# Kernel optimization log

Hardware: AMD Instinct MI355X
Metric: run time of the kernel (lower is better)

The kernel has to match this reference:

```python
import jax, jax.numpy as jnp
import numpy as np

E = 8          # num_experts
K = 2          # num_experts_per_tok
D = 1024       # d_model
F = 4096       # d_ff


def setup_inputs() -> dict:
    key = jax.random.key(0)
    k1, k2, k3, k4, k5 = jax.random.split(key, 5)
    s = 0.02
    return {
        "x": jax.random.normal(k1, (2, 2048, D), dtype=jnp.float32),
        "gate_w": jax.random.normal(k2, (D, E), dtype=jnp.float32) * s,
        "w1": jax.random.normal(k3, (E, D, F), dtype=jnp.float32) * s,
        "w2": jax.random.normal(k4, (E, F, D), dtype=jnp.float32) * s,
        "w3": jax.random.normal(k5, (E, D, F), dtype=jnp.float32) * s,
    }


def reference(x, gate_w, w1, w2, w3):
    # x: [B, S, D] -> squash to tokens [T, D]
    xs = x.reshape(-1, x.shape[-1])                      # [T, D]
    gate_logits = xs @ gate_w                            # [T, E]
    topw, sel = jax.lax.top_k(gate_logits, K)            # [T, K] each
    # softmax over the K selected logits in float32, cast back (matches torch code)
    topw = jax.nn.softmax(topw.astype(jnp.float32), axis=-1).astype(x.dtype)
    # per-token combine weight for every expert: zero where not selected [T, E]
    comb = (jax.nn.one_hot(sel, E, dtype=x.dtype) * topw[..., None]).sum(axis=1)
    out = jnp.zeros_like(xs)
    # loop over fixed small expert count (structurally distinct weights);
    # masked-dense combine is mathematically identical to the gather/scatter
    # in the original (weight is exactly 0 for unselected tokens)
    for i in range(E):
        h = jax.nn.silu(xs @ w1[i]) * (xs @ w3[i])       # [T, F] SwiGLU
        out = out + comb[:, i:i + 1] * (h @ w2[i])       # [T, D]
    return out.reshape(x.shape)
```

## Files before the change

### kernel.cpp

```cpp
#include <hip/hip_runtime.h>


#define T_TOK 4096
#define DM    1024
#define FF    4096
#define NE    8

#define BM 128
#define BN 128
#define BK 32
#define BS 36

typedef unsigned short u16;
typedef short short8 __attribute__((ext_vector_type(8)));
typedef float floatx4 __attribute__((ext_vector_type(4)));

#define WS_COUNTS  0u
#define WS_CURS    32u
#define WS_OFFS    64u
#define WS_SEL     4096u
#define WS_SELW    (4096u + 32768u)
#define WS_STOK    (4096u + 65536u)
#define WS_SW      (4096u + 98304u)
#define WS_XBF     (1u << 20)
#define WS_HBUF    ((1u << 20) + (8u << 20))

__device__ __forceinline__ u16 f2bf(float f) {
  union { float f; unsigned int u; } v; v.f = f;
  unsigned int r = v.u + 0x7fffu + ((v.u >> 16) & 1u);
  return (u16)(r >> 16);
}

__device__ __forceinline__ short8 ld_b_frag(const u16* p) {
  union { unsigned long long q[2]; short8 v; } r;
  r.q[0] = *(const unsigned long long*)(p);
  r.q[1] = *(const unsigned long long*)(p + 4);
  return r.v;
}

__global__ __launch_bounds__(256) void gate_kernel(
    const float* __restrict__ x, const float* __restrict__ gw,
    u16* __restrict__ xbf, int* __restrict__ sel, float* __restrict__ selw,
    int* __restrict__ counts)
{
  const int t = blockIdx.x * 4 + (threadIdx.x >> 6);
  const int lane = threadIdx.x & 63;
  const float* xr = x + (size_t)t * DM;
  double acc[NE];
#pragma unroll
  for (int e = 0; e < NE; ++e) acc[e] = 0.0;
#pragma unroll 4
  for (int i = 0; i < 16; ++i) {
    const int d = i * 64 + lane;
    const float xv = xr[d];
    xbf[(size_t)t * DM + d] = f2bf(xv);
    const float4* g = (const float4*)(gw + (size_t)d * NE);
    float4 g0 = g[0], g1 = g[1];
    acc[0] += (double)xv * g0.x; acc[1] += (double)xv * g0.y;
    acc[2] += (double)xv * g0.z; acc[3] += (double)xv * g0.w;
    acc[4] += (double)xv * g1.x; acc[5] += (double)xv * g1.y;
    acc[6] += (double)xv * g1.z; acc[7] += (double)xv * g1.w;
  }
#pragma unroll
  for (int off = 32; off >= 1; off >>= 1) {
#pragma unroll
    for (int e = 0; e < NE; ++e) acc[e] += __shfl_xor(acc[e], off, 64);
  }
  if (lane == 0) {
    int i1 = 0; double v1 = acc[0];
#pragma unroll
    for (int e = 1; e < NE; ++e) if (acc[e] > v1) { v1 = acc[e]; i1 = e; }
    int i2 = -1; double v2 = -1e300;
#pragma unroll
    for (int e = 0; e < NE; ++e) if (e != i1 && acc[e] > v2) { v2 = acc[e]; i2 = e; }
    float p1 = 1.0f / (1.0f + expf((float)(v2 - v1)));
    sel[t * 2] = i1; sel[t * 2 + 1] = i2;
    selw[t * 2] = p1; selw[t * 2 + 1] = 1.0f - p1;
    atomicAdd(&counts[i1], 1);
    atomicAdd(&counts[i2], 1);
  }
}

__global__ void offsets_kernel(const int* __restrict__ counts, int* __restrict__ offsets) {
  if (threadIdx.x == 0) {
    int s = 0;
#pragma unroll
    for (int e = 0; e < NE; ++e) { offsets[e] = s; s += counts[e]; }
  }
}

__global__ void fill_kernel(const int* __restrict__ sel, const float* __restrict__ selw,
                            const int* __restrict__ offsets, int* __restrict__ cursors,
                            int* __restrict__ stok, float* __restrict__ sw)
{
  const int t = blockIdx.x * blockDim.x + threadIdx.x;
  if (t >= T_TOK) return;
#pragma unroll
  for (int k = 0; k < 2; ++k) {
    int e = sel[t * 2 + k];
    int pos = atomicAdd(&cursors[e], 1);
    int p = offsets[e] + pos;
    stok[p] = t;
    sw[p] = selw[t * 2 + k];
  }
}

__global__ __launch_bounds__(256, 2) void gemm1_kernel(
    const u16* __restrict__ xbf, const float* __restrict__ w1, const float* __restrict__ w3,
    const int* __restrict__ stok, const int* __restrict__ offsets,
    const int* __restrict__ counts, u16* __restrict__ Hbuf)
{
  const int e  = blockIdx.z;
  const int mt = blockIdx.y;
  const int ne = counts[e];
  if (mt * BM >= ne) return;
  const int nt = blockIdx.x;
  const int base = offsets[e];
  const float* __restrict__ W1 = w1 + (size_t)e * DM * FF;
  const float* __restrict__ W3 = w3 + (size_t)e * DM * FF;

  __shared__ u16 Al[BM][BK];
  __shared__ u16 B1l[BN][BS];
  __shared__ u16 B3l[BN][BS];

  const int tid  = threadIdx.x;
  const int lane = tid & 63;
  const int wv   = tid >> 6;
  const int wm   = (wv & 1) * 64;
  const int wn   = (wv >> 1) * 64;
  const int ln15 = lane & 15;
  const int q    = lane >> 4;

  const int arow = tid >> 1;
  const int aseg = (tid & 1) * 16;
  const int rg_a = mt * BM + arow;
  const u16* asrc = nullptr;
  if (rg_a < ne) {
    int tok = stok[base + rg_a];
    asrc = xbf + (size_t)tok * DM + aseg;
  }

  const int nb = tid & 127;
  const int kh = (tid >> 7) * 16;
  const int n0 = nt * BN;
  const float* b1p = W1 + (size_t)kh * FF + n0 + nb;
  const float* b3p = W3 + (size_t)kh * FF + n0 + nb;

  floatx4 acc1[4][4], acc3[4][4];
#pragma unroll
  for (int mi = 0; mi < 4; ++mi)
#pragma unroll
    for (int ni = 0; ni < 4; ++ni) {
      acc1[mi][ni] = (floatx4){0.f, 0.f, 0.f, 0.f};
      acc3[mi][ni] = (floatx4){0.f, 0.f, 0.f, 0.f};
    }

  for (int kc = 0; kc < DM; kc += BK) {
    if (asrc) {
      const uint4* s = (const uint4*)(asrc + kc);
      *(uint4*)&Al[arow][aseg]     = s[0];
      *(uint4*)&Al[arow][aseg + 8] = s[1];
    } else {
      uint4 z = {0u, 0u, 0u, 0u};
      *(uint4*)&Al[arow][aseg]     = z;
      *(uint4*)&Al[arow][aseg + 8] = z;
    }
    const float* p1 = b1p + (size_t)kc * FF;
    const float* p3 = b3p + (size_t)kc * FF;
#pragma unroll
    for (int kk = 0; kk < 16; kk += 4) {
      union { u16 s[4]; uint2 u; } v1, v3;
#pragma unroll
      for (int j = 0; j < 4; ++j) {
        v1.s[j] = f2bf(p1[(size_t)(kk + j) * FF]);
        v3.s[j] = f2bf(p3[(size_t)(kk + j) * FF]);
      }
      *(uint2*)&B1l[nb][kh + kk] = v1.u;
      *(uint2*)&B3l[nb][kh + kk] = v3.u;
    }
    __syncthreads();

    short8 af[4];
#pragma unroll
    for (int mi = 0; mi < 4; ++mi)
      af[mi] = *(const short8*)&Al[wm + mi * 16 + ln15][q * 8];
#pragma unroll
    for (int ni = 0; ni < 4; ++ni) {
      short8 b1 = ld_b_frag(&B1l[wn + ni * 16 + ln15][q * 8]);
      short8 b3 = ld_b_frag(&B3l[wn + ni * 16 + ln15][q * 8]);
#pragma unroll
      for (int mi = 0; mi < 4; ++mi) {
        acc1[mi][ni] = __builtin_amdgcn_mfma_f32_16x16x32_bf16(af[mi], b1, acc1[mi][ni], 0, 0, 0);
        acc3[mi][ni] = __builtin_amdgcn_mfma_f32_16x16x32_bf16(af[mi], b3, acc3[mi][ni], 0, 0, 0);
      }
    }
    __syncthreads();
  }

#pragma unroll
  for (int mi = 0; mi < 4; ++mi) {
#pragma unroll
    for (int reg = 0; reg < 4; ++reg) {
      int rg = mt * BM + wm + mi * 16 + q * 4 + reg;
      if (rg < ne) {
        u16* dst = Hbuf + (size_t)(base + rg) * FF + n0 + wn + ln15;
#pragma unroll
        for (int ni = 0; ni < 4; ++ni) {
          float a = acc1[mi][ni][reg];
          float b = acc3[mi][ni][reg];
          float h = (a / (1.0f + __expf(-a))) * b;
          dst[ni * 16] = f2bf(h);
        }
      }
    }
  }
}

__global__ __launch_bounds__(256, 2) void gemm2_kernel(
    const u16* __restrict__ Hbuf, const float* __restrict__ w2,
    const int* __restrict__ stok, const float* __restrict__ sw,
    const int* __restrict__ offsets, const int* __restrict__ counts,
    float* __restrict__ out)
{
  const int e  = blockIdx.z;
  const int mt = blockIdx.y;
  const int ne = counts[e];
  if (mt * BM >= ne) return;
  const int nt = blockIdx.x;
  const int base = offsets[e];
  const float* __restrict__ W2 = w2 + (size_t)e * FF * DM;

  __shared__ u16 Al[BM][BK];
  __shared__ u16 Bl[BN][BS];

  const int tid  = threadIdx.x;
  const int lane = tid & 63;
  const int wv   = tid >> 6;
  const int wm   = (wv & 1) * 64;
  const int wn   = (wv >> 1) * 64;
  const int ln15 = lane & 15;
  const int q    = lane >> 4;

  const int arow = tid >> 1;
  const int aseg = (tid & 1) * 16;
  const int rg_a = mt * BM + arow;
  const u16* asrc = nullptr;
  if (rg_a < ne) asrc = Hbuf + (size_t)(base + rg_a) * FF + aseg;

  const int nb = tid & 127;
  const int kh = (tid >> 7) * 16;
  const int n0 = nt * BN;
  const float* bp = W2 + (size_t)kh * DM + n0 + nb;

  floatx4 acc[4][4];
#pragma unroll
  for (int mi = 0; mi < 4; ++mi)
#pragma unroll
    for (int ni = 0; ni < 4; ++ni) acc[mi][ni] = (floatx4){0.f, 0.f, 0.f, 0.f};

  for (int kc = 0; kc < FF; kc += BK) {
    if (asrc) {
      const uint4* s = (const uint4*)(asrc + kc);
      *(uint4*)&Al[arow][aseg]     = s[0];
      *(uint4*)&Al[arow][aseg + 8] = s[1];
    } else {
      uint4 z = {0u, 0u, 0u, 0u};
      *(uint4*)&Al[arow][aseg]     = z;
      *(uint4*)&Al[arow][aseg + 8] = z;
    }
    const float* p2 = bp + (size_t)kc * DM;
#pragma unroll
    for (int kk = 0; kk < 16; kk += 4) {
      union { u16 s[4]; uint2 u; } v2;
#pragma unroll
      for (int j = 0; j < 4; ++j) v2.s[j] = f2bf(p2[(size_t)(kk + j) * DM]);
      *(uint2*)&Bl[nb][kh + kk] = v2.u;
    }
    __syncthreads();

    short8 af[4];
#pragma unroll
    for (int mi = 0; mi < 4; ++mi)
      af[mi] = *(const short8*)&Al[wm + mi * 16 + ln15][q * 8];
#pragma unroll
    for (int ni = 0; ni < 4; ++ni) {
      short8 b = ld_b_frag(&Bl[wn + ni * 16 + ln15][q * 8]);
#pragma unroll
      for (int mi = 0; mi < 4; ++mi)
        acc[mi][ni] = __builtin_amdgcn_mfma_f32_16x16x32_bf16(af[mi], b, acc[mi][ni], 0, 0, 0);
    }
    __syncthreads();
  }

#pragma unroll
  for (int mi = 0; mi < 4; ++mi) {
#pragma unroll
    for (int reg = 0; reg < 4; ++reg) {
      int rg = mt * BM + wm + mi * 16 + q * 4 + reg;
      if (rg < ne) {
        int p = base + rg;
        int tok = stok[p];
        float wgt = sw[p];
        float* dst = out + (size_t)tok * DM + n0 + wn + ln15;
#pragma unroll
        for (int ni = 0; ni < 4; ++ni)
          atomicAdd(&dst[ni * 16], wgt * acc[mi][ni][reg]);
      }
    }
  }
}

extern "C" void kernel_launch(void* const* d_in, const int* in_sizes, int n_in,
                              void* d_out, int out_size, void* d_ws, size_t ws_size,
                              hipStream_t stream) {
  const float* x  = (const float*)d_in[0];
  const float* gw = (const float*)d_in[1];
  const float* w1 = (const float*)d_in[2];
  const float* w2 = (const float*)d_in[3];
  const float* w3 = (const float*)d_in[4];
  float* out = (float*)d_out;
  char* ws = (char*)d_ws;

  int*   counts  = (int*)(ws + WS_COUNTS);
  int*   cursors = (int*)(ws + WS_CURS);
  int*   offsets = (int*)(ws + WS_OFFS);
  int*   sel     = (int*)(ws + WS_SEL);
  float* selw    = (float*)(ws + WS_SELW);
  int*   stok    = (int*)(ws + WS_STOK);
  float* sw      = (float*)(ws + WS_SW);
  u16*   xbf     = (u16*)(ws + WS_XBF);
  u16*   Hbuf    = (u16*)(ws + WS_HBUF);

  size_t need = (size_t)WS_HBUF + (size_t)(T_TOK * 2) * FF * 2;
  if (ws_size < need) return;

  hipMemsetAsync(ws, 0, 96, stream);
  hipMemsetAsync(d_out, 0, (size_t)T_TOK * DM * sizeof(float), stream);

  gate_kernel<<<T_TOK / 4, 256, 0, stream>>>(x, gw, xbf, sel, selw, counts);
  offsets_kernel<<<1, 64, 0, stream>>>(counts, offsets);
  fill_kernel<<<T_TOK / 256, 256, 0, stream>>>(sel, selw, offsets, cursors, stok, sw);
  gemm1_kernel<<<dim3(FF / BN, T_TOK / BM, NE), 256, 0, stream>>>(xbf, w1, w3, stok, offsets, counts, Hbuf);
  gemm2_kernel<<<dim3(DM / BN, T_TOK / BM, NE), 256, 0, stream>>>(Hbuf, w2, stok, sw, offsets, counts, out);
}
```

Measured before the change: 1.050 ms.

## Pre-transpose weights to bf16 and stream tiles via async global-to-LDS loads

Adds a conversion pass that transposes and casts w1, w3 and w2 to bf16 K-major layouts in the workspace each call. New GEMM kernels then copy A and B tiles straight into LDS with global_load_lds, with no per-thread fp32-to-bf16 conversion or transposed staging. The aim is to halve weight bytes read inside the GEMMs and simplify the load path. The cost is an extra read of all fp32 weights plus a bf16 write every call. The new loop also has no double buffering and may have LDS bank conflicts. The old path is kept as a fallback when the workspace is too small.

```diff
diff --git a/kernel.cpp b/kernel.cpp
--- a/kernel.cpp
+++ b/kernel.cpp
@@ -22,13 +22,22 @@
 #define WS_SELW    (4096u + 32768u)
 #define WS_STOK    (4096u + 65536u)
 #define WS_SW      (4096u + 98304u)
-#define WS_XBF     (1u << 20)
-#define WS_HBUF    ((1u << 20) + (8u << 20))
+#define WS_XBF     ((size_t)1 << 20)
+#define WS_HBUF    ((size_t)9 << 20)
+#define WS_WT1     ((size_t)73 << 20)
+#define WS_WT3     ((size_t)137 << 20)
+#define WS_WT2     ((size_t)201 << 20)
 
 __device__ __forceinline__ u16 f2bf(float f) {
   union { float f; unsigned int u; } v; v.f = f;
   unsigned int r = v.u + 0x7fffu + ((v.u >> 16) & 1u);
   return (u16)(r >> 16);
+}
+
+__device__ __forceinline__ void async16(u16* lds, const u16* g) {
+  __builtin_amdgcn_global_load_lds(
+      (const __attribute__((address_space(1))) unsigned int*)g,
+      (__attribute__((address_space(3))) unsigned int*)lds, 16, 0, 0);
 }
 
 __device__ __forceinline__ short8 ld_b_frag(const u16* p) {
@@ -105,6 +114,215 @@
   }
 }
 
+__global__ __launch_bounds__(256) void convt_kernel(const float* __restrict__ src,
+                                                    u16* __restrict__ dst, int K, int N)
+{
+  __shared__ float tile[64][65];
+  const int e = blockIdx.z;
+  src += (size_t)e * K * N;
+  dst += (size_t)e * K * N;
+  const int n0 = blockIdx.x * 64;
+  const int k0 = blockIdx.y * 64;
+  const int tr = threadIdx.x >> 4;
+  const int tc = (threadIdx.x & 15) * 4;
+#pragma unroll
+  for (int i = 0; i < 64; i += 16) {
+    const float4 v = *(const float4*)&src[(size_t)(k0 + tr + i) * N + n0 + tc];
+    tile[tr + i][tc]     = v.x; tile[tr + i][tc + 1] = v.y;
+    tile[tr + i][tc + 2] = v.z; tile[tr + i][tc + 3] = v.w;
+  }
+  __syncthreads();
+#pragma unroll
+  for (int i = 0; i < 64; i += 16) {
+    union { u16 s[4]; uint2 u; } o;
+#pragma unroll
+    for (int j = 0; j < 4; ++j) o.s[j] = f2bf(tile[tc + j][tr + i]);
+    *(uint2*)&dst[(size_t)(n0 + tr + i) * K + k0 + tc] = o.u;
+  }
+}
+
+__global__ __launch_bounds__(256, 2) void gemm1p_kernel(
+    const u16* __restrict__ xbf, const u16* __restrict__ wt1, const u16* __restrict__ wt3,
+    const int* __restrict__ stok, const int* __restrict__ offsets,
+    const int* __restrict__ counts, u16* __restrict__ Hbuf)
+{
+  const int e  = blockIdx.z;
+  const int mt = blockIdx.y;
+  const int ne = counts[e];
+  if (mt * BM >= ne) return;
+  const int nt = blockIdx.x;
+  const int base = offsets[e];
+  const u16* __restrict__ W1 = wt1 + (size_t)e * DM * FF;
+  const u16* __restrict__ W3 = wt3 + (size_t)e * DM * FF;
+
+  __shared__ u16 Al[BM * BK];
+  __shared__ u16 B1l[BN * BK];
+  __shared__ u16 B3l[BN * BK];
+
+  const int tid  = threadIdx.x;
+  const int lane = tid & 63;
+  const int wv   = tid >> 6;
+  const int wm   = (wv & 1) * 64;
+  const int wn   = (wv >> 1) * 64;
+  const int ln15 = lane & 15;
+  const int q    = lane >> 4;
+  const int n0   = nt * BN;
+
+  const int rsub = lane >> 2;
+  const int seg  = (lane & 3) * 8;
+
+  const u16* ag[2]; const u16* b1g[2]; const u16* b3g[2];
+#pragma unroll
+  for (int it = 0; it < 2; ++it) {
+    int r  = wv * 32 + it * 16 + rsub;
+    int rg = mt * BM + r;
+    int p  = base + (rg < ne ? rg : 0);
+    int tok = stok[p];
+    ag[it]  = xbf + (size_t)tok * DM + seg;
+    int n   = n0 + r;
+    b1g[it] = W1 + (size_t)n * DM + seg;
+    b3g[it] = W3 + (size_t)n * DM + seg;
+  }
+  u16* al[2]  = { Al  + (wv * 32) * BK, Al  + (wv * 32 + 16) * BK };
+  u16* b1l[2] = { B1l + (wv * 32) * BK, B1l + (wv * 32 + 16) * BK };
+  u16* b3l[2] = { B3l + (wv * 32) * BK, B3l + (wv * 32 + 16) * BK };
+
+  floatx4 acc1[4][4], acc3[4][4];
+#pragma unroll
+  for (int mi = 0; mi < 4; ++mi)
+#pragma unroll
+    for (int ni = 0; ni < 4; ++ni) {
+      acc1[mi][ni] = (floatx4){0.f, 0.f, 0.f, 0.f};
+      acc3[mi][ni] = (floatx4){0.f, 0.f, 0.f, 0.f};
+    }
+
+  for (int kc = 0; kc < DM; kc += BK) {
+    async16(al[0],  ag[0]  + kc); async16(al[1],  ag[1]  + kc);
+    async16(b1l[0], b1g[0] + kc); async16(b1l[1], b1g[1] + kc);
+    async16(b3l[0], b3g[0] + kc); async16(b3l[1], b3g[1] + kc);
+    __syncthreads();
+
+    short8 af[4];
+#pragma unroll
+    for (int mi = 0; mi < 4; ++mi)
+      af[mi] = *(const short8*)&Al[(wm + mi * 16 + ln15) * BK + q * 8];
+#pragma unroll
+    for (int ni = 0; ni < 4; ++ni) {
+      short8 f1 = *(const short8*)&B1l[(wn + ni * 16 + ln15) * BK + q * 8];
+      short8 f3 = *(const short8*)&B3l[(wn + ni * 16 + ln15) * BK + q * 8];
+#pragma unroll
+      for (int mi = 0; mi < 4; ++mi) {
+        acc1[mi][ni] = __builtin_amdgcn_mfma_f32_16x16x32_bf16(af[mi], f1, acc1[mi][ni], 0, 0, 0);
+        acc3[mi][ni] = __builtin_amdgcn_mfma_f32_16x16x32_bf16(af[mi], f3, acc3[mi][ni], 0, 0, 0);
+      }
+    }
+    __syncthreads();
+  }
+
+#pragma unroll
+  for (int mi = 0; mi < 4; ++mi) {
+#pragma unroll
+    for (int reg = 0; reg < 4; ++reg) {
+      int rg = mt * BM + wm + mi * 16 + q * 4 + reg;
+      if (rg < ne) {
+        u16* dst = Hbuf + (size_t)(base + rg) * FF + n0 + wn + ln15;
+#pragma unroll
+        for (int ni = 0; ni < 4; ++ni) {
+          float a = acc1[mi][ni][reg];
+          float b = acc3[mi][ni][reg];
+          float h = (a / (1.0f + __expf(-a))) * b;
+          dst[ni * 16] = f2bf(h);
+        }
+      }
+    }
+  }
+}
+
+__global__ __launch_bounds__(256, 2) void gemm2p_kernel(
+    const u16* __restrict__ Hbuf, const u16* __restrict__ wt2,
+    const int* __restrict__ stok, const float* __restrict__ sw,
+    const int* __restrict__ offsets, const int* __restrict__ counts,
+    float* __restrict__ out)
+{
+  const int e  = blockIdx.z;
+  const int mt = blockIdx.y;
+  const int ne = counts[e];
+  if (mt * BM >= ne) return;
+  const int nt = blockIdx.x;
+  const int base = offsets[e];
+  const u16* __restrict__ W2 = wt2 + (size_t)e * FF * DM;
+
+  __shared__ u16 Al[BM * BK];
+  __shared__ u16 Bl[BN * BK];
+
+  const int tid  = threadIdx.x;
+  const int lane = tid & 63;
+  const int wv   = tid >> 6;
+  const int wm   = (wv & 1) * 64;
+  const int wn   = (wv >> 1) * 64;
+  const int ln15 = lane & 15;
+  const int q    = lane >> 4;
+  const int n0   = nt * BN;
+
+  const int rsub = lane >> 2;
+  const int seg  = (lane & 3) * 8;
+
+  const u16* ag[2]; const u16* bg[2];
+#pragma unroll
+  for (int it = 0; it < 2; ++it) {
+    int r  = wv * 32 + it * 16 + rsub;
+    int rg = mt * BM + r;
+    int p  = base + (rg < ne ? rg : 0);
+    ag[it] = Hbuf + (size_t)p * FF + seg;
+    int n  = n0 + r;
+    bg[it] = W2 + (size_t)n * FF + seg;
+  }
+  u16* al[2] = { Al + (wv * 32) * BK, Al + (wv * 32 + 16) * BK };
+  u16* bl[2] = { Bl + (wv * 32) * BK, Bl + (wv * 32 + 16) * BK };
+
+  floatx4 acc[4][4];
+#pragma unroll
+  for (int mi = 0; mi < 4; ++mi)
+#pragma unroll
+    for (int ni = 0; ni < 4; ++ni) acc[mi][ni] = (floatx4){0.f, 0.f, 0.f, 0.f};
+
+  for (int kc = 0; kc < FF; kc += BK) {
+    async16(al[0], ag[0] + kc); async16(al[1], ag[1] + kc);
+    async16(bl[0], bg[0] + kc); async16(bl[1], bg[1] + kc);
+    __syncthreads();
+
+    short8 af[4];
+#pragma unroll
+    for (int mi = 0; mi < 4; ++mi)
+      af[mi] = *(const short8*)&Al[(wm + mi * 16 + ln15) * BK + q * 8];
+#pragma unroll
+    for (int ni = 0; ni < 4; ++ni) {
+      short8 bf = *(const short8*)&Bl[(wn + ni * 16 + ln15) * BK + q * 8];
+#pragma unroll
+      for (int mi = 0; mi < 4; ++mi)
+        acc[mi][ni] = __builtin_amdgcn_mfma_f32_16x16x32_bf16(af[mi], bf, acc[mi][ni], 0, 0, 0);
+    }
+    __syncthreads();
+  }
+
+#pragma unroll
+  for (int mi = 0; mi < 4; ++mi) {
+#pragma unroll
+    for (int reg = 0; reg < 4; ++reg) {
+      int rg = mt * BM + wm + mi * 16 + q * 4 + reg;
+      if (rg < ne) {
+        int p = base + rg;
+        int tok = stok[p];
+        float wgt = sw[p];
+        float* dst = out + (size_t)tok * DM + n0 + wn + ln15;
+#pragma unroll
+        for (int ni = 0; ni < 4; ++ni)
+          atomicAdd(&dst[ni * 16], wgt * acc[mi][ni][reg]);
+      }
+    }
+  }
+}
+
 __global__ __launch_bounds__(256, 2) void gemm1_kernel(
     const u16* __restrict__ xbf, const float* __restrict__ w1, const float* __restrict__ w3,
     const int* __restrict__ stok, const int* __restrict__ offsets,
@@ -331,8 +549,9 @@
   u16*   xbf     = (u16*)(ws + WS_XBF);
   u16*   Hbuf    = (u16*)(ws + WS_HBUF);
 
-  size_t need = (size_t)WS_HBUF + (size_t)(T_TOK * 2) * FF * 2;
-  if (ws_size < need) return;
+  const size_t need_full = (size_t)265 << 20;
+  const size_t need_min  = WS_HBUF + (size_t)(T_TOK * 2) * FF * 2;
+  if (ws_size < need_min) return;
 
   hipMemsetAsync(ws, 0, 96, stream);
   hipMemsetAsync(d_out, 0, (size_t)T_TOK * DM * sizeof(float), stream);
@@ -340,6 +559,22 @@
   gate_kernel<<<T_TOK / 4, 256, 0, stream>>>(x, gw, xbf, sel, selw, counts);
   offsets_kernel<<<1, 64, 0, stream>>>(counts, offsets);
   fill_kernel<<<T_TOK / 256, 256, 0, stream>>>(sel, selw, offsets, cursors, stok, sw);
-  gemm1_kernel<<<dim3(FF / BN, T_TOK / BM, NE), 256, 0, stream>>>(xbf, w1, w3, stok, offsets, counts, Hbuf);
-  gemm2_kernel<<<dim3(DM / BN, T_TOK / BM, NE), 256, 0, stream>>>(Hbuf, w2, stok, sw, offsets, counts, out);
-}
+
+  if (ws_size >= need_full) {
+    u16* Wt1 = (u16*)(ws + WS_WT1);
+    u16* Wt3 = (u16*)(ws + WS_WT3);
+    u16* Wt2 = (u16*)(ws + WS_WT2);
+    convt_kernel<<<dim3(FF / 64, DM / 64, NE), 256, 0, stream>>>(w1, Wt1, DM, FF);
+    convt_kernel<<<dim3(FF / 64, DM / 64, NE), 256, 0, stream>>>(w3, Wt3, DM, FF);
+    convt_kernel<<<dim3(DM / 64, FF / 64, NE), 256, 0, stream>>>(w2, Wt2, FF, DM);
+    gemm1p_kernel<<<dim3(FF / BN, T_TOK / BM, NE), 256, 0, stream>>>(
+        xbf, Wt1, Wt3, stok, offsets, counts, Hbuf);
+    gemm2p_kernel<<<dim3(DM / BN, T_TOK / BM, NE), 256, 0, stream>>>(
+        Hbuf, Wt2, stok, sw, offsets, counts, out);
+  } else {
+    gemm1_kernel<<<dim3(FF / BN, T_TOK / BM, NE), 256, 0, stream>>>(
+        xbf, w1, w3, stok, offsets, counts, Hbuf);
+    gemm2_kernel<<<dim3(DM / BN, T_TOK / BM, NE), 256, 0, stream>>>(
+        Hbuf, w2, stok, sw, offsets, counts, out);
+  }
+}
```

Measured after the change: 925.5 us. 11.9% less time.
